# Kernel tuning notes

Hardware: AMD Instinct MI355X
Metric: run time of the kernel (lower is better)

The kernel has to match this reference:

```python
import jax, jax.numpy as jnp
import numpy as np

K = 3  # involution kernel size


def dwconv3x3(x, w, b):
    # x: [B,C,H,W], w: [C,1,3,3] (depthwise, groups=C), b: [C]
    y = jax.lax.conv_general_dilated(
        x, w, window_strides=(1, 1), padding='SAME',
        dimension_numbers=('NCHW', 'OIHW', 'NCHW'),
        feature_group_count=x.shape[1])
    return y + b[None, :, None, None]


def conv1x1(x, w, b):
    # x: [B,C,H,W], w: [O,C], b: [O]
    return jnp.einsum('oc,bchw->bohw', w, x) + b[None, :, None, None]


def extract_patches(x):
    # x: [B,C,H,W] -> [B,C,K*K,H,W], zero-padded 'same' 3x3 neighborhoods
    B, C, H, W = x.shape
    p = (K - 1) // 2
    xp = jnp.pad(x, ((0, 0), (0, 0), (p, p), (p, p)))
    return jnp.stack([xp[:, :, i:i + H, j:j + W]
                      for i in range(K) for j in range(K)], axis=2)


def involution(x, w_red, b_red, w_span, b_span):
    # dynamic per-pixel kernels: [B, K*K, H, W]
    kern = conv1x1(jax.nn.relu(conv1x1(x, w_red, b_red)), w_span, b_span)
    patches = extract_patches(x)                 # [B,C,KK,H,W]
    return jnp.einsum('bkhw,bckhw->bchw', kern, patches)


def setup_inputs() -> dict:
    key = jax.random.key(0)
    ks = jax.random.split(key, 10)
    dim, red = 256, 64  # reduction ratio 4
    B, H, W = 8, 64, 64
    s = 0.05
    return {
        'x': jax.random.normal(ks[0], (B, dim, H, W), jnp.float32),
        'w_in': jax.random.normal(ks[1], (dim, 1, 3, 3), jnp.float32) * s,
        'b_in': jax.random.normal(ks[2], (dim,), jnp.float32) * s,
        'w_red': jax.random.normal(ks[3], (red, dim), jnp.float32) * s,
        'b_red': jax.random.normal(ks[4], (red,), jnp.float32) * s,
        'w_span': jax.random.normal(ks[5], (K * K, red), jnp.float32) * s,
        'b_span': jax.random.normal(ks[6], (K * K,), jnp.float32) * s,
        'w_out': jax.random.normal(ks[7], (dim, 1, 3, 3), jnp.float32) * s,
        'b_out': jax.random.normal(ks[8], (dim,), jnp.float32) * s,
    }


def reference(x, w_in, b_in, w_red, b_red, w_span, b_span, w_out, b_out):
    x = dwconv3x3(x, w_in, b_in)
    x = involution(x, w_red, b_red, w_span, b_span)
    x = dwconv3x3(x, w_out, b_out)
    return x
```

## Files before the change

### kernel.cpp

```cpp
#include <hip/hip_runtime.h>

#define BB 8
#define CC 256
#define HH 64
#define WW 64
#define RED 64
#define HW 4096
#define AST 72
#define XST 40
#define LSH 72
#define WLS 10

typedef __attribute__((ext_vector_type(8))) short s8v;
typedef __attribute__((ext_vector_type(4))) float f4v;

__device__ __forceinline__ unsigned short f2bf(float f) {
    unsigned u = __float_as_uint(f);
    u += 0x7fff + ((u >> 16) & 1);
    return (unsigned short)(u >> 16);
}
__device__ __forceinline__ float b2f(unsigned short u) {
    return __uint_as_float(((unsigned)u) << 16);
}

__global__ __launch_bounds__(256) void build_wtf(const float* __restrict__ w_red,
                                                 unsigned short* __restrict__ wtf) {
    int e = blockIdx.x * 256 + threadIdx.x;
    int j = e & 7, l = (e >> 3) & 63, nt = (e >> 9) & 3, kbg = e >> 11;
    int o = nt * 16 + (l & 15);
    int c = kbg * 32 + ((l >> 4) & 3) * 8 + j;
    wtf[e] = f2bf(w_red[o * CC + c]);
}

__global__ __launch_bounds__(256, 4) void dw_kern(const float* __restrict__ x,
                                                  const float* __restrict__ w_in,
                                                  const float* __restrict__ b_in,
                                                  const unsigned short* __restrict__ wtf,
                                                  const float* __restrict__ b_red,
                                                  const float* __restrict__ w_span,
                                                  const float* __restrict__ b_span,
                                                  float* __restrict__ kern,
                                                  unsigned short* __restrict__ x1g) {
    alignas(16) __shared__ char smem[8448 + 5120 + 10240 + 2640];
    unsigned short* xs  = (unsigned short*)smem;
    float* r_lds        = (float*)smem;
    unsigned short* xst = (unsigned short*)(smem + 8448);
    float* wl           = (float*)(smem + 13568);
    float* part         = (float*)(smem + 13568);
    float* ws_l         = (float*)(smem + 23808);
    float* br_l         = ws_l + 576;
    float* bs_l         = br_l + 64;

    const int t    = threadIdx.x;
    const int bx   = blockIdx.x;
    const int band = bx & 7;
    const int idx  = bx >> 3;
    const int h    = band * 8 + (idx >> 1);
    const int wh   = idx & 1;
    const int b    = blockIdx.y;
    const int l  = t & 63;
    const int wv = t >> 6;
    const int mt = wv & 1, nh = wv >> 1;
    const int m0 = mt << 4;
    const int q  = t & 7;
    const int pl = q << 2;
    const int wg = (wh << 5) | pl;
    const int cr = t >> 3;

    #pragma unroll
    for (int j = 0; j < 9; j++) {
        int i = j * 256 + t;
        wl[(i / 9) * WLS + (i % 9)] = w_in[i];
    }
    wl[t * WLS + 9] = b_in[t];
    ws_l[t]       = w_span[t];
    ws_l[256 + t] = w_span[256 + t];
    if (t < 64) { ws_l[512 + t] = w_span[512 + t]; br_l[t] = b_red[t]; }
    if (t < 9)  bs_l[t] = b_span[t];

    float4 pv[2][3]; float phal[2][3];

    auto loadX = [&](int c0) {
        #pragma unroll
        for (int s = 0; s < 2; s++) {
            const int cc = c0 + s * 32 + cr;
            const float* xp = x + ((size_t)(b * CC + cc)) * HW;
            #pragma unroll
            for (int ky = 0; ky < 3; ky++) {
                int hh = h + ky - 1;
                if (hh < 0 || hh >= HH) {
                    pv[s][ky] = make_float4(0.f, 0.f, 0.f, 0.f);
                    phal[s][ky] = 0.f;
                    continue;
                }
                const float* row = xp + hh * WW + wg;
                pv[s][ky] = *(const float4*)row;
                float hv = 0.f;
                if (q == 0) { if (wg > 0) hv = row[-1]; }
                else if (q == 7) { if (wg + 4 < WW) hv = row[4]; }
                phal[s][ky] = hv;
            }
        }
    };
    auto computeA = [&](int c0) {
        #pragma unroll
        for (int s = 0; s < 2; s++) {
            const int cl = s * 32 + cr;
            const int cc = c0 + cl;
            const float* wp = wl + cc * WLS;
            const float bb = wp[9];
            float4 a4 = make_float4(bb, bb, bb, bb);
            #pragma unroll
            for (int ky = 0; ky < 3; ky++) {
                float4 v = pv[s][ky];
                float lf = __shfl_up(v.w, 1);
                if (q == 0) lf = phal[s][ky];
                float rt = __shfl_down(v.x, 1);
                if (q == 7) rt = phal[s][ky];
                float k0 = wp[ky * 3 + 0], k1 = wp[ky * 3 + 1], k2 = wp[ky * 3 + 2];
                a4.x = fmaf(k0, lf,  a4.x); a4.y = fmaf(k0, v.x, a4.y);
                a4.z = fmaf(k0, v.y, a4.z); a4.w = fmaf(k0, v.z, a4.w);
                a4.x = fmaf(k1, v.x, a4.x); a4.y = fmaf(k1, v.y, a4.y);
                a4.z = fmaf(k1, v.z, a4.z); a4.w = fmaf(k1, v.w, a4.w);
                a4.x = fmaf(k2, v.y, a4.x); a4.y = fmaf(k2, v.z, a4.y);
                a4.z = fmaf(k2, v.w, a4.z); a4.w = fmaf(k2, rt,  a4.w);
            }
            ushort4 pk;
            pk.x = f2bf(a4.x); pk.y = f2bf(a4.y);
            pk.z = f2bf(a4.z); pk.w = f2bf(a4.w);
            xs[(pl + 0) * AST + cl] = pk.x;
            xs[(pl + 1) * AST + cl] = pk.y;
            xs[(pl + 2) * AST + cl] = pk.z;
            xs[(pl + 3) * AST + cl] = pk.w;
            *(ushort4*)&xst[cl * XST + pl] = pk;
        }
    };

    s8v bfr[2][2];
    auto loadB = [&](int k) {
        #pragma unroll
        for (int kb = 0; kb < 2; kb++)
            #pragma unroll
            for (int ntl = 0; ntl < 2; ntl++) {
                int nt = (nh << 1) + ntl;
                int kbg = (k << 1) + kb;
                bfr[kb][ntl] = *(const s8v*)(wtf + (((kbg * 4 + nt) * 64 + l) << 3));
            }
    };

    f4v acc[2] = {{0.f, 0.f, 0.f, 0.f}, {0.f, 0.f, 0.f, 0.f}};
    int4 x1r[4];
    const int c2  = t >> 2;
    const int px2 = (t & 3) << 3;

    loadX(0); loadB(0);
    __syncthreads();
    for (int k = 0; k < 4; k++) {
        computeA(k << 6);
        if (k < 3) loadX((k + 1) << 6);
        __syncthreads();
        #pragma unroll
        for (int kb = 0; kb < 2; kb++) {
            const unsigned short* ap =
                xs + (m0 + (l & 15)) * AST + (kb << 5) + ((l >> 4) & 3) * 8;
            s8v av = *(const s8v*)ap;
            #pragma unroll
            for (int ntl = 0; ntl < 2; ntl++)
                acc[ntl] = __builtin_amdgcn_mfma_f32_16x16x32_bf16(
                    av, bfr[kb][ntl], acc[ntl], 0, 0, 0);
        }
        x1r[k] = *(const int4*)&xst[c2 * XST + px2];
        if (k < 3) loadB(k + 1);
        __syncthreads();
    }

    #pragma unroll
    for (int ntl = 0; ntl < 2; ntl++) {
        int o = ((nh << 1) + ntl) * 16 + (l & 15);
        int pxr = m0 + ((l >> 4) & 3) * 4;
        #pragma unroll
        for (int i = 0; i < 4; i++)
            r_lds[o * 33 + pxr + i] = acc[ntl][i];
    }
    __syncthreads();

    const int px = t & 31;
    const int og = t >> 5;
    const int o0 = og << 3;
    float kk[9];
    #pragma unroll
    for (int j = 0; j < 9; j++) kk[j] = 0.f;
    #pragma unroll
    for (int i = 0; i < 8; i++) {
        float r = fmaxf(r_lds[(o0 + i) * 33 + px] + br_l[o0 + i], 0.f);
        #pragma unroll
        for (int j = 0; j < 9; j++) kk[j] = fmaf(ws_l[j * 64 + o0 + i], r, kk[j]);
    }
    __syncthreads();
    #pragma unroll
    for (int j = 0; j < 9; j++) part[(og * 9 + j) * 32 + px] = kk[j];
    __syncthreads();

    float* kp = kern + (size_t)b * 9 * HW + h * WW + (wh << 5) + px;
    const int jj = t >> 5;
    {
        float s = bs_l[jj];
        #pragma unroll
        for (int g = 0; g < 8; g++) s += part[(g * 9 + jj) * 32 + px];
        kp[jj * HW] = s;
    }
    if (t < 32) {
        float s = bs_l[8];
        #pragma unroll
        for (int g = 0; g < 8; g++) s += part[(g * 9 + 8) * 32 + px];
        kp[8 * HW] = s;
    }

    #pragma unroll
    for (int k = 0; k < 4; k++) {
        unsigned short* dst = x1g + ((size_t)(b * CC + (k << 6) + c2)) * HW
                            + h * WW + (wh << 5) + px2;
        *(int4*)dst = x1r[k];
    }
}

__global__ __launch_bounds__(256, 8) void invol_dw(const unsigned short* __restrict__ x1g,
                                                   const float* __restrict__ kern,
                                                   const float* __restrict__ w_out,
                                                   const float* __restrict__ b_out,
                                                   float* __restrict__ out) {
    __shared__ unsigned short x1s[HH * LSH];
    __shared__ unsigned short res[HH * LSH];
    const int t  = threadIdx.x;
    const int q  = t & 15;
    const int w0 = q << 2;
    const int r  = t >> 4;
    const int c = blockIdx.x, b = blockIdx.y;

    {
        const unsigned short* xp = x1g + ((size_t)(b * CC + c)) * HW;
        const int hl = t >> 2;
        const int wl2 = (t & 3) << 4;
        *(s8v*)&x1s[hl * LSH + wl2]     = *(const s8v*)(xp + hl * WW + wl2);
        *(s8v*)&x1s[hl * LSH + wl2 + 8] = *(const s8v*)(xp + hl * WW + wl2 + 8);
    }
    __syncthreads();

    const float* kp = kern + (size_t)b * 9 * HW;
    #pragma unroll
    for (int i = 0; i < 4; i++) {
        int h  = r + (i << 4);
        int hw = h * WW + w0;
        float4 acc = make_float4(0.f, 0.f, 0.f, 0.f);
        #pragma unroll
        for (int ky = 0; ky < 3; ky++) {
            int hh = h + ky - 1;
            if (hh < 0 || hh >= HH) continue;
            const unsigned short* row = &x1s[hh * LSH + w0];
            float vx = b2f(row[0]), vy = b2f(row[1]);
            float vz = b2f(row[2]), vw = b2f(row[3]);
            float lf = (w0 > 0)      ? b2f(row[-1]) : 0.f;
            float rt = (w0 + 4 < WW) ? b2f(row[4])  : 0.f;
            float4 k0 = *(const float4*)(kp + (ky * 3 + 0) * HW + hw);
            float4 k1 = *(const float4*)(kp + (ky * 3 + 1) * HW + hw);
            float4 k2 = *(const float4*)(kp + (ky * 3 + 2) * HW + hw);
            acc.x = fmaf(k0.x, lf, acc.x); acc.y = fmaf(k0.y, vx, acc.y);
            acc.z = fmaf(k0.z, vy, acc.z); acc.w = fmaf(k0.w, vz, acc.w);
            acc.x = fmaf(k1.x, vx, acc.x); acc.y = fmaf(k1.y, vy, acc.y);
            acc.z = fmaf(k1.z, vz, acc.z); acc.w = fmaf(k1.w, vw, acc.w);
            acc.x = fmaf(k2.x, vy, acc.x); acc.y = fmaf(k2.y, vz, acc.y);
            acc.z = fmaf(k2.z, vw, acc.z); acc.w = fmaf(k2.w, rt, acc.w);
        }
        ushort4 pk;
        pk.x = f2bf(acc.x); pk.y = f2bf(acc.y);
        pk.z = f2bf(acc.z); pk.w = f2bf(acc.w);
        *(ushort4*)&res[h * LSH + w0] = pk;
    }
    __syncthreads();

    const float* wp = w_out + c * 9;
    const float bb = b_out[c];
    float* op = out + ((size_t)(b * CC + c)) * HW;
    #pragma unroll
    for (int i = 0; i < 4; i++) {
        int h = r + (i << 4);
        float4 acc = make_float4(bb, bb, bb, bb);
        #pragma unroll
        for (int ky = 0; ky < 3; ky++) {
            int hh = h + ky - 1;
            if (hh < 0 || hh >= HH) continue;
            const unsigned short* row = &res[hh * LSH + w0];
            float vx = b2f(row[0]), vy = b2f(row[1]);
            float vz = b2f(row[2]), vw = b2f(row[3]);
            float lf = (w0 > 0)      ? b2f(row[-1]) : 0.f;
            float rt = (w0 + 4 < WW) ? b2f(row[4])  : 0.f;
            float k0 = wp[ky * 3 + 0], k1 = wp[ky * 3 + 1], k2 = wp[ky * 3 + 2];
            acc.x = fmaf(k0, lf, acc.x); acc.y = fmaf(k0, vx, acc.y);
            acc.z = fmaf(k0, vy, acc.z); acc.w = fmaf(k0, vz, acc.w);
            acc.x = fmaf(k1, vx, acc.x); acc.y = fmaf(k1, vy, acc.y);
            acc.z = fmaf(k1, vz, acc.z); acc.w = fmaf(k1, vw, acc.w);
            acc.x = fmaf(k2, vy, acc.x); acc.y = fmaf(k2, vz, acc.y);
            acc.z = fmaf(k2, vw, acc.z); acc.w = fmaf(k2, rt, acc.w);
        }
        *(float4*)(op + h * WW + w0) = acc;
    }
}

extern "C" void kernel_launch(void* const* d_in, const int* in_sizes, int n_in,
                              void* d_out, int out_size, void* d_ws, size_t ws_size,
                              hipStream_t stream) {
    const float* x      = (const float*)d_in[0];
    const float* w_in   = (const float*)d_in[1];
    const float* b_in   = (const float*)d_in[2];
    const float* w_red  = (const float*)d_in[3];
    const float* b_red  = (const float*)d_in[4];
    const float* w_span = (const float*)d_in[5];
    const float* b_span = (const float*)d_in[6];
    const float* w_out  = (const float*)d_in[7];
    const float* b_out  = (const float*)d_in[8];
    float* out = (float*)d_out;

    float* kern = (float*)d_ws;
    unsigned short* x1g = (unsigned short*)(kern + (size_t)BB * 9 * HW);
    unsigned short* wtf = x1g + (size_t)BB * CC * HW;

    build_wtf<<<64, 256, 0, stream>>>(w_red, wtf);
    dw_kern<<<dim3(128, BB), 256, 0, stream>>>(x, w_in, b_in, wtf, b_red,
                                               w_span, b_span, kern, x1g);
    invol_dw<<<dim3(CC, BB), 256, 0, stream>>>(x1g, kern, w_out, b_out, out);
}
```

Before: 143.0 us.

## Fuse weight prep, dwconv/kernel-gen and involution stages into one flag-synced kernel

Merges the three launches into a single grid. Blocks spin on global release/acquire flags so that weight conversion finishes before the MFMA stage and all spatial tiles of a batch finish before the involution plus output dwconv. Each block then handles two channels in the last phase. This removes two launch boundaries and their tail gaps. The cost is that the whole grid must be co-resident or it can deadlock, the last phase runs at half the previous block count, and the MAGIC flags are never reset, so later calls skip the waits and can read stale intermediates.

```diff
diff --git a/kernel.cpp b/kernel.cpp
--- a/kernel.cpp
+++ b/kernel.cpp
@@ -10,6 +10,7 @@
 #define XST 40
 #define LSH 72
 #define WLS 10
+#define MAGIC 0x5A6B7C8Du
 
 typedef __attribute__((ext_vector_type(8))) short s8v;
 typedef __attribute__((ext_vector_type(4))) float f4v;
@@ -22,26 +23,27 @@
 __device__ __forceinline__ float b2f(unsigned short u) {
     return __uint_as_float(((unsigned)u) << 16);
 }
-
-__global__ __launch_bounds__(256) void build_wtf(const float* __restrict__ w_red,
-                                                 unsigned short* __restrict__ wtf) {
-    int e = blockIdx.x * 256 + threadIdx.x;
-    int j = e & 7, l = (e >> 3) & 63, nt = (e >> 9) & 3, kbg = e >> 11;
-    int o = nt * 16 + (l & 15);
-    int c = kbg * 32 + ((l >> 4) & 3) * 8 + j;
-    wtf[e] = f2bf(w_red[o * CC + c]);
-}
-
-__global__ __launch_bounds__(256, 4) void dw_kern(const float* __restrict__ x,
-                                                  const float* __restrict__ w_in,
-                                                  const float* __restrict__ b_in,
-                                                  const unsigned short* __restrict__ wtf,
-                                                  const float* __restrict__ b_red,
-                                                  const float* __restrict__ w_span,
-                                                  const float* __restrict__ b_span,
-                                                  float* __restrict__ kern,
-                                                  unsigned short* __restrict__ x1g) {
-    alignas(16) __shared__ char smem[8448 + 5120 + 10240 + 2640];
+__device__ __forceinline__ void waitFlag(unsigned* p) {
+    while (__hip_atomic_load(p, __ATOMIC_ACQUIRE, __HIP_MEMORY_SCOPE_AGENT) != MAGIC)
+        __builtin_amdgcn_s_sleep(2);
+}
+
+__global__ __launch_bounds__(256, 4) void fused(const float* __restrict__ x,
+                                                const float* __restrict__ w_in,
+                                                const float* __restrict__ b_in,
+                                                const float* __restrict__ w_red,
+                                                const float* __restrict__ b_red,
+                                                const float* __restrict__ w_span,
+                                                const float* __restrict__ b_span,
+                                                const float* __restrict__ w_out,
+                                                const float* __restrict__ b_out,
+                                                float* __restrict__ out,
+                                                float* __restrict__ kern,
+                                                unsigned short* __restrict__ x1g,
+                                                unsigned short* __restrict__ wtf,
+                                                unsigned* __restrict__ flw,
+                                                unsigned* __restrict__ fld) {
+    alignas(16) __shared__ char smem[26448];
     unsigned short* xs  = (unsigned short*)smem;
     float* r_lds        = (float*)smem;
     unsigned short* xst = (unsigned short*)(smem + 8448);
@@ -53,11 +55,25 @@
 
     const int t    = threadIdx.x;
     const int bx   = blockIdx.x;
+    const int b    = blockIdx.y;
+
+    if (b == 0 && bx < 64) {
+        int e = bx * 256 + t;
+        int j = e & 7, l2 = (e >> 3) & 63, nt = (e >> 9) & 3, kbg = e >> 11;
+        int o = nt * 16 + (l2 & 15);
+        int c = kbg * 32 + ((l2 >> 4) & 3) * 8 + j;
+        wtf[e] = f2bf(w_red[o * CC + c]);
+        __threadfence();
+        __syncthreads();
+        if (t == 0)
+            __hip_atomic_store(&flw[bx], MAGIC, __ATOMIC_RELEASE,
+                               __HIP_MEMORY_SCOPE_AGENT);
+    }
+
     const int band = bx & 7;
     const int idx  = bx >> 3;
     const int h    = band * 8 + (idx >> 1);
     const int wh   = idx & 1;
-    const int b    = blockIdx.y;
     const int l  = t & 63;
     const int wv = t >> 6;
     const int mt = wv & 1, nh = wv >> 1;
@@ -153,8 +169,10 @@
     const int c2  = t >> 2;
     const int px2 = (t & 3) << 3;
 
-    loadX(0); loadB(0);
-    __syncthreads();
+    loadX(0);
+    if (t < 64) waitFlag(&flw[t]);
+    __syncthreads();
+    loadB(0);
     for (int k = 0; k < 4; k++) {
         computeA(k << 6);
         if (k < 3) loadX((k + 1) << 6);
@@ -222,87 +240,93 @@
                             + h * WW + (wh << 5) + px2;
         *(int4*)dst = x1r[k];
     }
-}
-
-__global__ __launch_bounds__(256, 8) void invol_dw(const unsigned short* __restrict__ x1g,
-                                                   const float* __restrict__ kern,
-                                                   const float* __restrict__ w_out,
-                                                   const float* __restrict__ b_out,
-                                                   float* __restrict__ out) {
-    __shared__ unsigned short x1s[HH * LSH];
-    __shared__ unsigned short res[HH * LSH];
-    const int t  = threadIdx.x;
-    const int q  = t & 15;
-    const int w0 = q << 2;
-    const int r  = t >> 4;
-    const int c = blockIdx.x, b = blockIdx.y;
-
-    {
-        const unsigned short* xp = x1g + ((size_t)(b * CC + c)) * HW;
-        const int hl = t >> 2;
-        const int wl2 = (t & 3) << 4;
-        *(s8v*)&x1s[hl * LSH + wl2]     = *(const s8v*)(xp + hl * WW + wl2);
-        *(s8v*)&x1s[hl * LSH + wl2 + 8] = *(const s8v*)(xp + hl * WW + wl2 + 8);
-    }
-    __syncthreads();
-
-    const float* kp = kern + (size_t)b * 9 * HW;
-    #pragma unroll
-    for (int i = 0; i < 4; i++) {
-        int h  = r + (i << 4);
-        int hw = h * WW + w0;
-        float4 acc = make_float4(0.f, 0.f, 0.f, 0.f);
-        #pragma unroll
-        for (int ky = 0; ky < 3; ky++) {
-            int hh = h + ky - 1;
-            if (hh < 0 || hh >= HH) continue;
-            const unsigned short* row = &x1s[hh * LSH + w0];
-            float vx = b2f(row[0]), vy = b2f(row[1]);
-            float vz = b2f(row[2]), vw = b2f(row[3]);
-            float lf = (w0 > 0)      ? b2f(row[-1]) : 0.f;
-            float rt = (w0 + 4 < WW) ? b2f(row[4])  : 0.f;
-            float4 k0 = *(const float4*)(kp + (ky * 3 + 0) * HW + hw);
-            float4 k1 = *(const float4*)(kp + (ky * 3 + 1) * HW + hw);
-            float4 k2 = *(const float4*)(kp + (ky * 3 + 2) * HW + hw);
-            acc.x = fmaf(k0.x, lf, acc.x); acc.y = fmaf(k0.y, vx, acc.y);
-            acc.z = fmaf(k0.z, vy, acc.z); acc.w = fmaf(k0.w, vz, acc.w);
-            acc.x = fmaf(k1.x, vx, acc.x); acc.y = fmaf(k1.y, vy, acc.y);
-            acc.z = fmaf(k1.z, vz, acc.z); acc.w = fmaf(k1.w, vw, acc.w);
-            acc.x = fmaf(k2.x, vy, acc.x); acc.y = fmaf(k2.y, vz, acc.y);
-            acc.z = fmaf(k2.z, vw, acc.z); acc.w = fmaf(k2.w, rt, acc.w);
-        }
-        ushort4 pk;
-        pk.x = f2bf(acc.x); pk.y = f2bf(acc.y);
-        pk.z = f2bf(acc.z); pk.w = f2bf(acc.w);
-        *(ushort4*)&res[h * LSH + w0] = pk;
-    }
-    __syncthreads();
-
-    const float* wp = w_out + c * 9;
-    const float bb = b_out[c];
-    float* op = out + ((size_t)(b * CC + c)) * HW;
-    #pragma unroll
-    for (int i = 0; i < 4; i++) {
-        int h = r + (i << 4);
-        float4 acc = make_float4(bb, bb, bb, bb);
-        #pragma unroll
-        for (int ky = 0; ky < 3; ky++) {
-            int hh = h + ky - 1;
-            if (hh < 0 || hh >= HH) continue;
-            const unsigned short* row = &res[hh * LSH + w0];
-            float vx = b2f(row[0]), vy = b2f(row[1]);
-            float vz = b2f(row[2]), vw = b2f(row[3]);
-            float lf = (w0 > 0)      ? b2f(row[-1]) : 0.f;
-            float rt = (w0 + 4 < WW) ? b2f(row[4])  : 0.f;
-            float k0 = wp[ky * 3 + 0], k1 = wp[ky * 3 + 1], k2 = wp[ky * 3 + 2];
-            acc.x = fmaf(k0, lf, acc.x); acc.y = fmaf(k0, vx, acc.y);
-            acc.z = fmaf(k0, vy, acc.z); acc.w = fmaf(k0, vz, acc.w);
-            acc.x = fmaf(k1, vx, acc.x); acc.y = fmaf(k1, vy, acc.y);
-            acc.z = fmaf(k1, vz, acc.z); acc.w = fmaf(k1, vw, acc.w);
-            acc.x = fmaf(k2, vy, acc.x); acc.y = fmaf(k2, vz, acc.y);
-            acc.z = fmaf(k2, vw, acc.z); acc.w = fmaf(k2, rt, acc.w);
-        }
-        *(float4*)(op + h * WW + w0) = acc;
+
+    __threadfence();
+    __syncthreads();
+    if (t == 0)
+        __hip_atomic_store(&fld[b * 128 + bx], MAGIC, __ATOMIC_RELEASE,
+                           __HIP_MEMORY_SCOPE_AGENT);
+
+    if (t < 128) waitFlag(&fld[b * 128 + t]);
+    __syncthreads();
+
+    unsigned short* x1s = (unsigned short*)smem;
+    unsigned short* res = (unsigned short*)(smem + 9216);
+    const int qi  = t & 15;
+    const int w0i = qi << 2;
+    const int ri  = t >> 4;
+    const float* kpb = kern + (size_t)b * 9 * HW;
+
+    for (int p = 0; p < 2; p++) {
+        const int c = (bx << 1) | p;
+
+        {
+            const unsigned short* xp = x1g + ((size_t)(b * CC + c)) * HW;
+            const int hl = t >> 2;
+            const int wl2 = (t & 3) << 4;
+            *(s8v*)&x1s[hl * LSH + wl2]     = *(const s8v*)(xp + hl * WW + wl2);
+            *(s8v*)&x1s[hl * LSH + wl2 + 8] = *(const s8v*)(xp + hl * WW + wl2 + 8);
+        }
+        __syncthreads();
+
+        #pragma unroll
+        for (int i = 0; i < 4; i++) {
+            int hq = ri + (i << 4);
+            int hw = hq * WW + w0i;
+            float4 a = make_float4(0.f, 0.f, 0.f, 0.f);
+            #pragma unroll
+            for (int ky = 0; ky < 3; ky++) {
+                int hh = hq + ky - 1;
+                if (hh < 0 || hh >= HH) continue;
+                const unsigned short* row = &x1s[hh * LSH + w0i];
+                float vx = b2f(row[0]), vy = b2f(row[1]);
+                float vz = b2f(row[2]), vw = b2f(row[3]);
+                float lf = (w0i > 0)      ? b2f(row[-1]) : 0.f;
+                float rt = (w0i + 4 < WW) ? b2f(row[4])  : 0.f;
+                float4 k0 = *(const float4*)(kpb + (ky * 3 + 0) * HW + hw);
+                float4 k1 = *(const float4*)(kpb + (ky * 3 + 1) * HW + hw);
+                float4 k2 = *(const float4*)(kpb + (ky * 3 + 2) * HW + hw);
+                a.x = fmaf(k0.x, lf, a.x); a.y = fmaf(k0.y, vx, a.y);
+                a.z = fmaf(k0.z, vy, a.z); a.w = fmaf(k0.w, vz, a.w);
+                a.x = fmaf(k1.x, vx, a.x); a.y = fmaf(k1.y, vy, a.y);
+                a.z = fmaf(k1.z, vz, a.z); a.w = fmaf(k1.w, vw, a.w);
+                a.x = fmaf(k2.x, vy, a.x); a.y = fmaf(k2.y, vz, a.y);
+                a.z = fmaf(k2.z, vw, a.z); a.w = fmaf(k2.w, rt, a.w);
+            }
+            ushort4 pk;
+            pk.x = f2bf(a.x); pk.y = f2bf(a.y);
+            pk.z = f2bf(a.z); pk.w = f2bf(a.w);
+            *(ushort4*)&res[hq * LSH + w0i] = pk;
+        }
+        __syncthreads();
+
+        const float* wp = w_out + c * 9;
+        const float bb = b_out[c];
+        float* op = out + ((size_t)(b * CC + c)) * HW;
+        #pragma unroll
+        for (int i = 0; i < 4; i++) {
+            int hq = ri + (i << 4);
+            float4 a = make_float4(bb, bb, bb, bb);
+            #pragma unroll
+            for (int ky = 0; ky < 3; ky++) {
+                int hh = hq + ky - 1;
+                if (hh < 0 || hh >= HH) continue;
+                const unsigned short* row = &res[hh * LSH + w0i];
+                float vx = b2f(row[0]), vy = b2f(row[1]);
+                float vz = b2f(row[2]), vw = b2f(row[3]);
+                float lf = (w0i > 0)      ? b2f(row[-1]) : 0.f;
+                float rt = (w0i + 4 < WW) ? b2f(row[4])  : 0.f;
+                float k0 = wp[ky * 3 + 0], k1 = wp[ky * 3 + 1], k2 = wp[ky * 3 + 2];
+                a.x = fmaf(k0, lf, a.x); a.y = fmaf(k0, vx, a.y);
+                a.z = fmaf(k0, vy, a.z); a.w = fmaf(k0, vz, a.w);
+                a.x = fmaf(k1, vx, a.x); a.y = fmaf(k1, vy, a.y);
+                a.z = fmaf(k1, vz, a.z); a.w = fmaf(k1, vw, a.w);
+                a.x = fmaf(k2, vy, a.x); a.y = fmaf(k2, vz, a.y);
+                a.z = fmaf(k2, vw, a.z); a.w = fmaf(k2, rt, a.w);
+            }
+            *(float4*)(op + hq * WW + w0i) = a;
+        }
+        __syncthreads();
     }
 }
 
@@ -323,9 +347,10 @@
     float* kern = (float*)d_ws;
     unsigned short* x1g = (unsigned short*)(kern + (size_t)BB * 9 * HW);
     unsigned short* wtf = x1g + (size_t)BB * CC * HW;
-
-    build_wtf<<<64, 256, 0, stream>>>(w_red, wtf);
-    dw_kern<<<dim3(128, BB), 256, 0, stream>>>(x, w_in, b_in, wtf, b_red,
-                                               w_span, b_span, kern, x1g);
-    invol_dw<<<dim3(CC, BB), 256, 0, stream>>>(x1g, kern, w_out, b_out, out);
-}
+    unsigned* flw = (unsigned*)(wtf + 16384);
+    unsigned* fld = flw + 64;
+
+    fused<<<dim3(128, BB), 256, 0, stream>>>(x, w_in, b_in, w_red, b_red,
+                                             w_span, b_span, w_out, b_out,
+                                             out, kern, x1g, wtf, flw, fld);
+}
```

After: 350.4 us. 2.45x slower.
